# Kernel tuning notes

Measured on AMD Instinct MI355X. Metric: run time of the kernel, lower is better.

## Reference

```python
import jax, jax.numpy as jnp
import numpy as np

H, KV, D = 16, 4, 128
EPS = 1e-6

def setup_inputs() -> dict:
    key = jax.random.key(0)
    ks = jax.random.split(key, 7)
    B, S, HS = 2, 2048, 2048
    return {
        "hidden_states": jax.random.normal(ks[0], (B, S, HS), jnp.float32),
        "cos": jax.random.uniform(ks[1], (S, D), jnp.float32),
        "sin": jax.random.uniform(ks[2], (S, D), jnp.float32),
        "Wq": jax.random.normal(ks[3], (H * D, HS), jnp.float32) * 0.02,
        "Wk": jax.random.normal(ks[4], (KV * D, HS), jnp.float32) * 0.02,
        "Wv": jax.random.normal(ks[5], (KV * D, HS), jnp.float32) * 0.02,
        "Wo": jax.random.normal(ks[6], (HS, H * D), jnp.float32) * 0.02,
        "norm_q_w": jnp.ones((D,), jnp.float32),
        "norm_k_w": jnp.ones((D,), jnp.float32),
    }

def _rmsnorm(x, w):
    # RMSNorm over head_dim
    return x * jax.lax.rsqrt(jnp.mean(x * x, axis=-1, keepdims=True) + EPS) * w

def _rope(x, cos, sin):
    # x: [B, S, heads, D]; cos/sin: [S, D]; rotate-half (use_real_unbind_dim=-2)
    c = cos[None, :, None, :]
    s = sin[None, :, None, :]
    x1, x2 = jnp.split(x, 2, axis=-1)
    x_rot = jnp.concatenate([-x2, x1], axis=-1)
    return x * c + x_rot * s

def reference(hidden_states, cos, sin, Wq, Wk, Wv, Wo, norm_q_w, norm_k_w):
    B, S, _ = hidden_states.shape
    q = (hidden_states @ Wq.T).reshape(B, S, H, D)
    k = (hidden_states @ Wk.T).reshape(B, S, KV, D)
    v = (hidden_states @ Wv.T).reshape(B, S, KV, D)
    q = _rmsnorm(q, norm_q_w)
    k = _rmsnorm(k, norm_k_w)
    q = _rope(q, cos, sin)
    k = _rope(k, cos, sin)
    # GQA: repeat_interleave K/V heads to match Q heads
    g = H // KV
    k = jnp.repeat(k, g, axis=2)  # [B, S, H, D]
    v = jnp.repeat(v, g, axis=2)
    scores = jnp.einsum('bqhd,bkhd->bhqk', q, k) * (D ** -0.5)
    attn = jax.nn.softmax(scores, axis=-1)
    out = jnp.einsum('bhqk,bkhd->bqhd', attn, v)  # [B, S, H, D]
    out = out.reshape(B, S, H * D)
    return out @ Wo.T
```

## Files before the change

### kernel.cpp

```cpp
#include <hip/hip_runtime.h>


typedef __attribute__((ext_vector_type(8))) short bf16x8;
typedef __attribute__((ext_vector_type(4))) float f32x4;
typedef __attribute__((ext_vector_type(16))) float f32x16;

__device__ __forceinline__ unsigned short f2bf(float x) {
  union { float f; unsigned u; } v; v.f = x;
  unsigned r = v.u + 0x7fffu + ((v.u >> 16) & 1u);
  return (unsigned short)(r >> 16);
}

__device__ __forceinline__ unsigned cvt_pk_bf16(float lo, float hi) {
  unsigned r;
  asm("v_cvt_pk_bf16_f32 %0, %1, %2" : "=v"(r) : "v"(lo), "v"(hi));
  return r;
}

__device__ __forceinline__ void gload_lds16(const void* g, void* l) {
  __builtin_amdgcn_global_load_lds(
      (const __attribute__((address_space(1))) void*)g,
      (__attribute__((address_space(3))) void*)l, 16, 0, 0);
}

__global__ __launch_bounds__(256) void cvt4(const float4* __restrict__ in,
                                            ushort4* __restrict__ out, int n4) {
  int i = blockIdx.x * 256 + threadIdx.x;
  if (i < n4) {
    float4 v = in[i];
    out[i] = make_ushort4(f2bf(v.x), f2bf(v.y), f2bf(v.z), f2bf(v.w));
  }
}

__global__ __launch_bounds__(256) void gemm_bt_f32(
    const unsigned short* __restrict__ A, const unsigned short* __restrict__ B,
    float* __restrict__ C, int M, int N, int K) {
  __shared__ unsigned short lsA[128 * 32];
  __shared__ unsigned short lsB[128 * 32];
  const int tid = threadIdx.x;
  const int wave = tid >> 6;
  const int lane = tid & 63;
  const int lrow = lane & 15;
  const int kg = lane >> 4;
  const int nbn = N >> 7;
  const int bm = blockIdx.x / nbn;
  const int bn = blockIdx.x % nbn;
  const int m0 = bm << 7, n0 = bn << 7;
  const int wm = (wave >> 1) << 6, wn = (wave & 1) << 6;
  const f32x4 zero = {0.f, 0.f, 0.f, 0.f};
  f32x4 acc[4][4];
#pragma unroll
  for (int i = 0; i < 4; ++i)
#pragma unroll
    for (int j = 0; j < 4; ++j) acc[i][j] = zero;
  const int srow = tid >> 2;
  const int scol = (tid & 3) << 3;

  for (int k0 = 0; k0 < K; k0 += 32) {
    __syncthreads();
    gload_lds16(A + (size_t)(m0 + srow) * K + k0 + scol, (char*)lsA + wave * 1024);
    gload_lds16(A + (size_t)(m0 + 64 + srow) * K + k0 + scol, (char*)lsA + 4096 + wave * 1024);
    gload_lds16(B + (size_t)(n0 + srow) * K + k0 + scol, (char*)lsB + wave * 1024);
    gload_lds16(B + (size_t)(n0 + 64 + srow) * K + k0 + scol, (char*)lsB + 4096 + wave * 1024);
    __syncthreads();
    bf16x8 fa[4], fb[4];
#pragma unroll
    for (int i = 0; i < 4; ++i) {
      fa[i] = *(const bf16x8*)(lsA + ((wm + i * 16 + lrow) << 5) + (kg << 3));
      fb[i] = *(const bf16x8*)(lsB + ((wn + i * 16 + lrow) << 5) + (kg << 3));
    }
#pragma unroll
    for (int i = 0; i < 4; ++i)
#pragma unroll
      for (int j = 0; j < 4; ++j)
        acc[i][j] = __builtin_amdgcn_mfma_f32_16x16x32_bf16(fa[i], fb[j], acc[i][j], 0, 0, 0);
  }
#pragma unroll
  for (int i = 0; i < 4; ++i) {
#pragma unroll
    for (int j = 0; j < 4; ++j) {
      int col = n0 + wn + j * 16 + lrow;
      int rbase = m0 + wm + i * 16 + kg * 4;
#pragma unroll
      for (int t = 0; t < 4; ++t)
        C[(size_t)(rbase + t) * N + col] = acc[i][j][t];
    }
  }
}

__global__ __launch_bounds__(256) void rms_rope(
    const float* __restrict__ QKV, const float* __restrict__ cosT,
    const float* __restrict__ sinT, const float* __restrict__ wq,
    const float* __restrict__ wk, unsigned short* __restrict__ Q,
    unsigned short* __restrict__ Kg, unsigned short* __restrict__ Vg) {
  int task = blockIdx.x * 4 + (threadIdx.x >> 6);
  int lane = threadIdx.x & 63;
  int row = task / 24;
  int slot = task - row * 24;
  int b = row >> 11, s = row & 2047;
  const float* x = QKV + (size_t)row * 3072 + slot * 128;
  float x1 = x[lane], x2 = x[lane + 64];
  if (slot < 20) {
    float ss = x1 * x1 + x2 * x2;
#pragma unroll
    for (int msk = 1; msk < 64; msk <<= 1) ss += __shfl_xor(ss, msk);
    float inv = rsqrtf(ss * (1.0f / 128.0f) + 1e-6f);
    const float* w = (slot < 16) ? wq : wk;
    x1 *= inv * w[lane];
    x2 *= inv * w[lane + 64];
    float c1 = cosT[s * 128 + lane], c2 = cosT[s * 128 + lane + 64];
    float sn1 = sinT[s * 128 + lane], sn2 = sinT[s * 128 + lane + 64];
    float o1 = x1 * c1 - x2 * sn1;
    float o2 = x2 * c2 + x1 * sn2;
    if (slot < 16) {
      const float qs = 0.08838834764831845f * 1.4426950408889634f;
      o1 *= qs; o2 *= qs;
    }
    x1 = o1; x2 = o2;
  }
  if (slot < 16) {
    unsigned short* dst = Q + (((size_t)b * 16 + slot) * 2048 + s) * 128;
    dst[lane] = f2bf(x1);
    dst[lane + 64] = f2bf(x2);
  } else {
    int kv = (slot - 16) & 3;
    size_t tb = ((size_t)((b * 4 + kv) * 32) + (s >> 6)) * 16384;
    int key = s & 63;
    if (slot < 20) {
      char* base = (char*)Kg + tb;
      int xr = (key & 7) << 4;
      *(unsigned short*)(base + key * 256 + ((lane * 2) ^ xr)) = f2bf(x1);
      *(unsigned short*)(base + key * 256 + (((lane + 64) * 2) ^ xr)) = f2bf(x2);
    } else {
      char* base = (char*)Vg + tb;
      int p = key >> 4;
      int vhi = (key >> 2) & 1;
      int e = (key & 3) | (((key >> 3) & 1) << 2);
      int off = p * 4096 + vhi * 512 + e * 2;
      int d1 = lane, d2 = lane + 64;
      *(unsigned short*)(base + off + (d1 >> 5) * 1024 + (d1 & 31) * 16) = f2bf(x1);
      *(unsigned short*)(base + off + (d2 >> 5) * 1024 + (d2 & 31) * 16) = f2bf(x2);
    }
  }
}

__global__ __launch_bounds__(256, 2) void attn64(
    const unsigned short* __restrict__ Q, const unsigned short* __restrict__ Kg,
    const unsigned short* __restrict__ Vg, unsigned short* __restrict__ O) {
  __shared__ unsigned short Kl[2][8192];
  __shared__ unsigned short Vl[2][8192];
  const int tid = threadIdx.x;
  const int wave = tid >> 6, lane = tid & 63;
  const int l31 = lane & 31, hi = lane >> 5;
  int bid = blockIdx.x;
  bid = (bid & 7) * 64 + (bid >> 3);
  const int bh = bid >> 4, qt = bid & 15;
  const int b = bh >> 4, h = bh & 15, kh = h >> 2;
  const char* Kt = (const char*)Kg + (size_t)(b * 4 + kh) * 524288;
  const char* Vt = (const char*)Vg + (size_t)(b * 4 + kh) * 524288;
  const unsigned short* Qb =
      Q + ((size_t)(b * 16 + h) * 2048 + qt * 128 + wave * 32) * 128;
  bf16x8 qf[8];
#pragma unroll
  for (int s = 0; s < 8; ++s)
    qf[s] = *(const bf16x8*)(Qb + l31 * 128 + s * 16 + hi * 8);
  f32x16 acc[4];
#pragma unroll
  for (int c = 0; c < 4; ++c)
#pragma unroll
    for (int r = 0; r < 16; ++r) acc[c][r] = 0.f;
  float m = -1e30f, lsum = 0.f;
  const int xrk = (l31 & 7) << 4;

  auto stage = [&](int t) {
    const char* kt = Kt + (size_t)t * 16384;
    const char* vt = Vt + (size_t)t * 16384;
    char* kd = (char*)Kl[t & 1];
    char* vd = (char*)Vl[t & 1];
#pragma unroll
    for (int c = 0; c < 4; ++c) {
      gload_lds16(kt + c * 4096 + tid * 16, kd + c * 4096 + wave * 1024);
      gload_lds16(vt + c * 4096 + tid * 16, vd + c * 4096 + wave * 1024);
    }
  };

  auto qk = [&](int t, f32x16& s0, f32x16& s1) {
    const char* Kb = (const char*)Kl[t & 1];
#pragma unroll
    for (int r = 0; r < 16; ++r) { s0[r] = 0.f; s1[r] = 0.f; }
#pragma unroll
    for (int s = 0; s < 8; ++s) {
      int xo = (s * 32 + hi * 16) ^ xrk;
      bf16x8 k0 = *(const bf16x8*)(Kb + l31 * 256 + xo);
      bf16x8 k1 = *(const bf16x8*)(Kb + (32 + l31) * 256 + xo);
      s0 = __builtin_amdgcn_mfma_f32_32x32x16_bf16(k0, qf[s], s0, 0, 0, 0);
      s1 = __builtin_amdgcn_mfma_f32_32x32x16_bf16(k1, qf[s], s1, 0, 0, 0);
    }
  };

  auto body = [&](int t, f32x16& c0, f32x16& c1, f32x16& n0, f32x16& n1) {
    float t8[8];
#pragma unroll
    for (int r = 0; r < 8; ++r)
      t8[r] = fmaxf(fmaxf(c0[r], c0[r + 8]), fmaxf(c1[r], c1[r + 8]));
#pragma unroll
    for (int r = 0; r < 4; ++r) t8[r] = fmaxf(t8[r], t8[r + 4]);
    float mx = fmaxf(fmaxf(t8[0], t8[1]), fmaxf(t8[2], t8[3]));
    mx = fmaxf(mx, __shfl_xor(mx, 32));
    if (__any(mx > m + 8.f)) {
      float mn = fmaxf(m, mx);
      float sc = exp2f(m - mn);
      m = mn;
      lsum *= sc;
#pragma unroll
      for (int r = 0; r < 16; ++r) {
        float scq = __shfl(sc, (r & 3) + 8 * (r >> 2) + 4 * hi);
#pragma unroll
        for (int c = 0; c < 4; ++c) acc[c][r] *= scq;
      }
    }
    float p0[16], p1[16];
#pragma unroll
    for (int r = 0; r < 16; ++r) {
      p0[r] = exp2f(c0[r] - m);
      p1[r] = exp2f(c1[r] - m);
    }
    float u8[8];
#pragma unroll
    for (int r = 0; r < 8; ++r) u8[r] = (p0[r] + p0[r + 8]) + (p1[r] + p1[r + 8]);
#pragma unroll
    for (int r = 0; r < 4; ++r) u8[r] += u8[r + 4];
    float sum = (u8[0] + u8[1]) + (u8[2] + u8[3]);
    sum += __shfl_xor(sum, 32);
    lsum += sum;
    union { bf16x8 v[4]; unsigned w[16]; } pa;
#pragma unroll
    for (int r = 0; r < 4; ++r) {
      pa.w[r]      = cvt_pk_bf16(p0[2 * r], p0[2 * r + 1]);
      pa.w[4 + r]  = cvt_pk_bf16(p0[8 + 2 * r], p0[9 + 2 * r]);
      pa.w[8 + r]  = cvt_pk_bf16(p1[2 * r], p1[2 * r + 1]);
      pa.w[12 + r] = cvt_pk_bf16(p1[8 + 2 * r], p1[9 + 2 * r]);
    }
    __syncthreads();
    __builtin_amdgcn_s_setprio(1);
    if (t + 1 < 32) qk(t + 1, n0, n1);
    const char* Vb = (const char*)Vl[t & 1];
#pragma unroll
    for (int p = 0; p < 4; ++p)
#pragma unroll
      for (int c = 0; c < 4; ++c) {
        bf16x8 vf = *(const bf16x8*)(Vb + p * 4096 + c * 1024 + hi * 512 + l31 * 16);
        acc[c] = __builtin_amdgcn_mfma_f32_32x32x16_bf16(pa.v[p], vf, acc[c], 0, 0, 0);
      }
    __builtin_amdgcn_s_setprio(0);
    __syncthreads();
    if (t + 2 < 32) stage(t + 2);
  };

  stage(0);
  __syncthreads();
  f32x16 s0A, s1A, s0B, s1B;
  qk(0, s0A, s1A);
  stage(1);

  for (int t = 0; t < 32; t += 2) {
    body(t, s0A, s1A, s0B, s1B);
    body(t + 1, s0B, s1B, s0A, s1A);
  }

  float inv = 1.0f / lsum;
#pragma unroll
  for (int r = 0; r < 16; ++r) {
    int q = (r & 3) + 8 * (r >> 2) + 4 * hi;
    float invq = __shfl(inv, q);
    int srow = qt * 128 + wave * 32 + q;
    unsigned short* dst = O + (((size_t)b * 2048 + srow) * 16 + h) * 128;
#pragma unroll
    for (int c = 0; c < 4; ++c)
      dst[c * 32 + l31] = f2bf(acc[c][r] * invq);
  }
}

extern "C" void kernel_launch(void* const* d_in, const int* in_sizes, int n_in,
                              void* d_out, int out_size, void* d_ws, size_t ws_size,
                              hipStream_t stream) {
  const float* hs   = (const float*)d_in[0];
  const float* cosT = (const float*)d_in[1];
  const float* sinT = (const float*)d_in[2];
  const float* Wq   = (const float*)d_in[3];
  const float* Wk   = (const float*)d_in[4];
  const float* Wv   = (const float*)d_in[5];
  const float* Wo   = (const float*)d_in[6];
  const float* nqw  = (const float*)d_in[7];
  const float* nkw  = (const float*)d_in[8];
  float* out = (float*)d_out;

  char* ws = (char*)d_ws;
  unsigned short* X    = (unsigned short*)ws;
  unsigned short* Wqkv = X + 8388608;
  unsigned short* WoB  = Wqkv + 6291456;
  float* QKV           = (float*)(WoB + 4194304);
  unsigned short* Qb   = (unsigned short*)(QKV + 12582912);
  unsigned short* Kg   = Qb + 8388608;
  unsigned short* Vg   = Kg + 2097152;
  unsigned short* Ob   = (unsigned short*)QKV;

  cvt4<<<8192, 256, 0, stream>>>((const float4*)hs, (ushort4*)X, 2097152);
  cvt4<<<4096, 256, 0, stream>>>((const float4*)Wq, (ushort4*)Wqkv, 1048576);
  cvt4<<<1024, 256, 0, stream>>>((const float4*)Wk, (ushort4*)(Wqkv + 4194304), 262144);
  cvt4<<<1024, 256, 0, stream>>>((const float4*)Wv, (ushort4*)(Wqkv + 5242880), 262144);
  cvt4<<<4096, 256, 0, stream>>>((const float4*)Wo, (ushort4*)WoB, 1048576);

  gemm_bt_f32<<<32 * 24, 256, 0, stream>>>(X, Wqkv, QKV, 4096, 3072, 2048);

  rms_rope<<<24576, 256, 0, stream>>>(QKV, cosT, sinT, nqw, nkw, Qb, Kg, Vg);

  attn64<<<512, 256, 0, stream>>>(Qb, Kg, Vg, Ob);

  gemm_bt_f32<<<32 * 16, 256, 0, stream>>>(Ob, WoB, out, 4096, 2048, 2048);
}
```

Baseline: 260.9 us.

## Use 256-row double-buffered GEMM, bf16 QKV output, and drop online softmax max

Replaces both projection GEMMs with a templated 512-thread kernel. It uses 256xBN tiles, XOR-swizzled LDS, two-stage double-buffered async global-to-LDS loads with explicit waitcnt/barrier scheduling, and a block-index remap. The QKV projection now writes bf16 instead of fp32, which halves intermediate traffic into rms_rope. The attention kernel stops tracking a running max and computes exp2 of the raw scores, removing the max reduction and rescaling. This depends on bounded logits from RMSNorm with the given norm weights and risks overflow for other weights.

```diff
diff --git a/kernel.cpp b/kernel.cpp
--- a/kernel.cpp
+++ b/kernel.cpp
@@ -9,6 +9,11 @@
   union { float f; unsigned u; } v; v.f = x;
   unsigned r = v.u + 0x7fffu + ((v.u >> 16) & 1u);
   return (unsigned short)(r >> 16);
+}
+
+__device__ __forceinline__ float bf2f(unsigned short h) {
+  union { unsigned u; float f; } v; v.u = (unsigned)h << 16;
+  return v.f;
 }
 
 __device__ __forceinline__ unsigned cvt_pk_bf16(float lo, float hi) {
@@ -32,64 +37,117 @@
   }
 }
 
-__global__ __launch_bounds__(256) void gemm_bt_f32(
-    const unsigned short* __restrict__ A, const unsigned short* __restrict__ B,
-    float* __restrict__ C, int M, int N, int K) {
-  __shared__ unsigned short lsA[128 * 32];
-  __shared__ unsigned short lsB[128 * 32];
+template <int NF, bool OUT_BF16>
+__global__ __launch_bounds__(512, 2) void gemm_bt_8ph(
+    const unsigned short* __restrict__ A, const unsigned short* __restrict__ Bm,
+    void* __restrict__ Cout, int M, int N, int K) {
+  __shared__ char lsA[2][32768];
+  __shared__ char lsB[2][NF * 8192];
   const int tid = threadIdx.x;
-  const int wave = tid >> 6;
-  const int lane = tid & 63;
-  const int lrow = lane & 15;
-  const int kg = lane >> 4;
-  const int nbn = N >> 7;
-  const int bm = blockIdx.x / nbn;
-  const int bn = blockIdx.x % nbn;
-  const int m0 = bm << 7, n0 = bn << 7;
-  const int wm = (wave >> 1) << 6, wn = (wave & 1) << 6;
-  const f32x4 zero = {0.f, 0.f, 0.f, 0.f};
-  f32x4 acc[4][4];
-#pragma unroll
-  for (int i = 0; i < 4; ++i)
-#pragma unroll
-    for (int j = 0; j < 4; ++j) acc[i][j] = zero;
+  const int wave = tid >> 6, lane = tid & 63;
+  const int lrow = lane & 15, kg = lane >> 4;
+  const int wm = wave >> 2, wn = wave & 3;
+  const int BN = NF * 64;
+  const int nbn = N / BN;
+  const int bid = (blockIdx.x & 7) * (gridDim.x >> 3) + (blockIdx.x >> 3);
+  const int m0 = (bid / nbn) << 8;
+  const int n0 = (bid % nbn) * BN;
+  const int NT = K >> 6;
+
   const int srow = tid >> 2;
-  const int scol = (tid & 3) << 3;
-
-  for (int k0 = 0; k0 < K; k0 += 32) {
-    __syncthreads();
-    gload_lds16(A + (size_t)(m0 + srow) * K + k0 + scol, (char*)lsA + wave * 1024);
-    gload_lds16(A + (size_t)(m0 + 64 + srow) * K + k0 + scol, (char*)lsA + 4096 + wave * 1024);
-    gload_lds16(B + (size_t)(n0 + srow) * K + k0 + scol, (char*)lsB + wave * 1024);
-    gload_lds16(B + (size_t)(n0 + 64 + srow) * K + k0 + scol, (char*)lsB + 4096 + wave * 1024);
-    __syncthreads();
-    bf16x8 fa[4], fb[4];
-#pragma unroll
-    for (int i = 0; i < 4; ++i) {
-      fa[i] = *(const bf16x8*)(lsA + ((wm + i * 16 + lrow) << 5) + (kg << 3));
-      fb[i] = *(const bf16x8*)(lsB + ((wn + i * 16 + lrow) << 5) + (kg << 3));
-    }
-#pragma unroll
-    for (int i = 0; i < 4; ++i)
-#pragma unroll
-      for (int j = 0; j < 4; ++j)
-        acc[i][j] = __builtin_amdgcn_mfma_f32_16x16x32_bf16(fa[i], fb[j], acc[i][j], 0, 0, 0);
-  }
-#pragma unroll
-  for (int i = 0; i < 4; ++i) {
-#pragma unroll
-    for (int j = 0; j < 4; ++j) {
-      int col = n0 + wn + j * 16 + lrow;
-      int rbase = m0 + wm + i * 16 + kg * 4;
-#pragma unroll
-      for (int t = 0; t < 4; ++t)
-        C[(size_t)(rbase + t) * N + col] = acc[i][j][t];
+  const int scol = (((tid & 3) ^ (srow & 3)) << 3);
+  const size_t a0 = (size_t)(m0 + srow) * K + scol;
+  const size_t a1 = (size_t)(m0 + 128 + srow) * K + scol;
+  const size_t b0 = (size_t)(n0 + srow) * K + scol;
+  const size_t b1 = (size_t)(n0 + 128 + srow) * K + scol;
+
+  f32x4 acc[8][NF];
+#pragma unroll
+  for (int i = 0; i < 8; ++i)
+#pragma unroll
+    for (int j = 0; j < NF; ++j)
+#pragma unroll
+      for (int t = 0; t < 4; ++t) acc[i][j][t] = 0.f;
+
+  const int xk = ((kg ^ (lrow & 3)) << 4);
+  const int abase = (wm * 128 + lrow) * 64 + xk;
+  const int bbase = (wn * NF * 16 + lrow) * 64 + xk;
+
+  auto stage_plane = [&](int T, int ks) {
+    if (T >= NT) return;
+    const int buf = T & 1;
+    const size_t kof = (size_t)T * 64 + ks * 32;
+    char* da = lsA[buf] + ks * 16384 + wave * 1024;
+    gload_lds16(A + a0 + kof, da);
+    gload_lds16(A + a1 + kof, da + 8192);
+    char* db = lsB[buf] + ks * (NF * 4096) + wave * 1024;
+    gload_lds16(Bm + b0 + kof, db);
+    if (NF >= 3) {
+      if (tid < 256) gload_lds16(Bm + b1 + kof, db + 8192);
+    }
+  };
+
+  auto phase = [&](int T, int ks, int sT, int sKs) {
+    const int buf = T & 1;
+    const char* pa = lsA[buf] + ks * 16384;
+    const char* pb = lsB[buf] + ks * (NF * 4096);
+    bf16x8 af[8], bfr[NF];
+#pragma unroll
+    for (int mf = 0; mf < 8; ++mf)
+      af[mf] = *(const bf16x8*)(pa + abase + mf * 1024);
+#pragma unroll
+    for (int nf = 0; nf < NF; ++nf)
+      bfr[nf] = *(const bf16x8*)(pb + bbase + nf * 1024);
+    stage_plane(sT, sKs);
+    asm volatile("s_waitcnt vmcnt(6)" ::: "memory");
+    __builtin_amdgcn_s_barrier();
+    asm volatile("s_waitcnt lgkmcnt(0)" ::: "memory");
+    __builtin_amdgcn_sched_barrier(0);
+    __builtin_amdgcn_s_setprio(1);
+#pragma unroll
+    for (int mf = 0; mf < 8; ++mf)
+#pragma unroll
+      for (int nf = 0; nf < NF; ++nf)
+        acc[mf][nf] =
+            __builtin_amdgcn_mfma_f32_16x16x32_bf16(af[mf], bfr[nf], acc[mf][nf], 0, 0, 0);
+    __builtin_amdgcn_s_setprio(0);
+    __builtin_amdgcn_s_barrier();
+  };
+
+  stage_plane(0, 0);
+  stage_plane(0, 1);
+  stage_plane(1, 0);
+  asm volatile("s_waitcnt vmcnt(6)" ::: "memory");
+  __builtin_amdgcn_s_barrier();
+
+  for (int kt = 0; kt < NT; ++kt) {
+    phase(kt, 0, kt + 1, 1);
+    phase(kt, 1, kt + 2, 0);
+  }
+
+#pragma unroll
+  for (int mf = 0; mf < 8; ++mf) {
+#pragma unroll
+    for (int nf = 0; nf < NF; ++nf) {
+      int row = m0 + wm * 128 + mf * 16 + kg * 4;
+      int col = n0 + wn * NF * 16 + nf * 16 + lrow;
+      if (OUT_BF16) {
+        unsigned short* C = (unsigned short*)Cout;
+#pragma unroll
+        for (int t = 0; t < 4; ++t)
+          C[(size_t)(row + t) * N + col] = f2bf(acc[mf][nf][t]);
+      } else {
+        float* C = (float*)Cout;
+#pragma unroll
+        for (int t = 0; t < 4; ++t)
+          C[(size_t)(row + t) * N + col] = acc[mf][nf][t];
+      }
     }
   }
 }
 
 __global__ __launch_bounds__(256) void rms_rope(
-    const float* __restrict__ QKV, const float* __restrict__ cosT,
+    const unsigned short* __restrict__ QKV, const float* __restrict__ cosT,
     const float* __restrict__ sinT, const float* __restrict__ wq,
     const float* __restrict__ wk, unsigned short* __restrict__ Q,
     unsigned short* __restrict__ Kg, unsigned short* __restrict__ Vg) {
@@ -98,8 +156,8 @@
   int row = task / 24;
   int slot = task - row * 24;
   int b = row >> 11, s = row & 2047;
-  const float* x = QKV + (size_t)row * 3072 + slot * 128;
-  float x1 = x[lane], x2 = x[lane + 64];
+  const unsigned short* x = QKV + (size_t)row * 3072 + slot * 128;
+  float x1 = bf2f(x[lane]), x2 = bf2f(x[lane + 64]);
   if (slot < 20) {
     float ss = x1 * x1 + x2 * x2;
 #pragma unroll
@@ -169,7 +227,7 @@
   for (int c = 0; c < 4; ++c)
 #pragma unroll
     for (int r = 0; r < 16; ++r) acc[c][r] = 0.f;
-  float m = -1e30f, lsum = 0.f;
+  float lsum = 0.f;
   const int xrk = (l31 & 7) << 4;
 
   auto stage = [&](int t) {
@@ -198,41 +256,19 @@
     }
   };
 
-  auto body = [&](int t, f32x16& c0, f32x16& c1, f32x16& n0, f32x16& n1) {
-    float t8[8];
-#pragma unroll
-    for (int r = 0; r < 8; ++r)
-      t8[r] = fmaxf(fmaxf(c0[r], c0[r + 8]), fmaxf(c1[r], c1[r + 8]));
-#pragma unroll
-    for (int r = 0; r < 4; ++r) t8[r] = fmaxf(t8[r], t8[r + 4]);
-    float mx = fmaxf(fmaxf(t8[0], t8[1]), fmaxf(t8[2], t8[3]));
-    mx = fmaxf(mx, __shfl_xor(mx, 32));
-    if (__any(mx > m + 8.f)) {
-      float mn = fmaxf(m, mx);
-      float sc = exp2f(m - mn);
-      m = mn;
-      lsum *= sc;
-#pragma unroll
-      for (int r = 0; r < 16; ++r) {
-        float scq = __shfl(sc, (r & 3) + 8 * (r >> 2) + 4 * hi);
-#pragma unroll
-        for (int c = 0; c < 4; ++c) acc[c][r] *= scq;
-      }
-    }
+  auto body = [&](int t, f32x16& c0, f32x16& c1, f32x16& n0_, f32x16& n1_) {
     float p0[16], p1[16];
 #pragma unroll
     for (int r = 0; r < 16; ++r) {
-      p0[r] = exp2f(c0[r] - m);
-      p1[r] = exp2f(c1[r] - m);
+      p0[r] = exp2f(c0[r]);
+      p1[r] = exp2f(c1[r]);
     }
     float u8[8];
 #pragma unroll
     for (int r = 0; r < 8; ++r) u8[r] = (p0[r] + p0[r + 8]) + (p1[r] + p1[r + 8]);
 #pragma unroll
     for (int r = 0; r < 4; ++r) u8[r] += u8[r + 4];
-    float sum = (u8[0] + u8[1]) + (u8[2] + u8[3]);
-    sum += __shfl_xor(sum, 32);
-    lsum += sum;
+    lsum += (u8[0] + u8[1]) + (u8[2] + u8[3]);
     union { bf16x8 v[4]; unsigned w[16]; } pa;
 #pragma unroll
     for (int r = 0; r < 4; ++r) {
@@ -243,7 +279,7 @@
     }
     __syncthreads();
     __builtin_amdgcn_s_setprio(1);
-    if (t + 1 < 32) qk(t + 1, n0, n1);
+    if (t + 1 < 32) qk(t + 1, n0_, n1_);
     const char* Vb = (const char*)Vl[t & 1];
 #pragma unroll
     for (int p = 0; p < 4; ++p)
@@ -268,6 +304,7 @@
     body(t + 1, s0B, s1B, s0A, s1A);
   }
 
+  lsum += __shfl_xor(lsum, 32);
   float inv = 1.0f / lsum;
 #pragma unroll
   for (int r = 0; r < 16; ++r) {
@@ -299,11 +336,11 @@
   unsigned short* X    = (unsigned short*)ws;
   unsigned short* Wqkv = X + 8388608;
   unsigned short* WoB  = Wqkv + 6291456;
-  float* QKV           = (float*)(WoB + 4194304);
-  unsigned short* Qb   = (unsigned short*)(QKV + 12582912);
+  unsigned short* QKVb = WoB + 4194304;
+  unsigned short* Qb   = QKVb + 12582912;
   unsigned short* Kg   = Qb + 8388608;
   unsigned short* Vg   = Kg + 2097152;
-  unsigned short* Ob   = (unsigned short*)QKV;
+  unsigned short* Ob   = QKVb;
 
   cvt4<<<8192, 256, 0, stream>>>((const float4*)hs, (ushort4*)X, 2097152);
   cvt4<<<4096, 256, 0, stream>>>((const float4*)Wq, (ushort4*)Wqkv, 1048576);
@@ -311,11 +348,11 @@
   cvt4<<<1024, 256, 0, stream>>>((const float4*)Wv, (ushort4*)(Wqkv + 5242880), 262144);
   cvt4<<<4096, 256, 0, stream>>>((const float4*)Wo, (ushort4*)WoB, 1048576);
 
-  gemm_bt_f32<<<32 * 24, 256, 0, stream>>>(X, Wqkv, QKV, 4096, 3072, 2048);
-
-  rms_rope<<<24576, 256, 0, stream>>>(QKV, cosT, sinT, nqw, nkw, Qb, Kg, Vg);
+  gemm_bt_8ph<3, true><<<256, 512, 0, stream>>>(X, Wqkv, QKVb, 4096, 3072, 2048);
+
+  rms_rope<<<24576, 256, 0, stream>>>(QKVb, cosT, sinT, nqw, nkw, Qb, Kg, Vg);
 
   attn64<<<512, 256, 0, stream>>>(Qb, Kg, Vg, Ob);
 
-  gemm_bt_f32<<<32 * 16, 256, 0, stream>>>(Ob, WoB, out, 4096, 2048, 2048);
-}
+  gemm_bt_8ph<2, false><<<256, 512, 0, stream>>>(Ob, WoB, out, 4096, 2048, 2048);
+}
```

Measured after the change: 225.7 us. 1.16x faster.
